# Performance work log

Hardware: AMD Instinct MI355X
Metric: run time of the kernel (lower is better)

The kernel has to match this reference:

```python
import jax, jax.numpy as jnp
import numpy as np

N = 64          # num_atoms
K = 2           # num_edge_types
VDIM = 32
EDIM = 32
HID = 64        # hard-coded n_hid in the module
B = 128         # num_sims
E = N * (N - 1)
_off = ~np.eye(N, dtype=bool)
SEND, RECV = [np.asarray(a) for a in np.where(_off)]  # edge e: node SEND[e] -> node RECV[e] (NRI: rel_send=rows, rel_rec=cols)
EPS = 1e-5  # torch BatchNorm1d default


def _mlp(x, W1, b1, W2, b2, gamma, beta):
    # NRI MLP: fc1 -> ELU -> fc2 -> ELU -> BatchNorm1d (training-mode batch stats over all but last dim)
    h = jax.nn.elu(x @ W1 + b1)
    o = jax.nn.elu(h @ W2 + b2)
    ax = tuple(range(o.ndim - 1))
    mu = o.mean(ax, keepdims=True)
    var = o.var(ax, keepdims=True)  # biased variance, as torch BN uses for normalization
    return gamma * (o - mu) * jax.lax.rsqrt(var + EPS) + beta


def setup_inputs():
    key = jax.random.key(0)
    ks = jax.random.split(key, 16)
    p = lambda k, shape: jax.random.normal(k, shape, jnp.float32) * 0.05
    return {
        "v0": jax.random.normal(ks[0], (B, N, VDIM), jnp.float32),
        "e0": jax.random.normal(ks[1], (B, N, N - 1, EDIM), jnp.float32),
        "edge_type": jax.random.uniform(ks[2], (B, E, K), dtype=jnp.float32),
        "mlpv_W1": p(ks[3], (EDIM, HID)), "mlpv_b1": p(ks[4], (HID,)),
        "mlpv_W2": p(ks[5], (HID, VDIM)), "mlpv_b2": p(ks[6], (VDIM,)),
        "mlpv_gamma": jnp.ones((VDIM,), jnp.float32), "mlpv_beta": jnp.zeros((VDIM,), jnp.float32),
        "mlpe_W1": p(ks[7], (K, 2 * VDIM, HID)), "mlpe_b1": p(ks[8], (K, HID)),
        "mlpe_W2": p(ks[9], (K, HID, EDIM)), "mlpe_b2": p(ks[10], (K, EDIM)),
        "mlpe_gamma": jnp.ones((K, EDIM), jnp.float32), "mlpe_beta": jnp.zeros((K, EDIM), jnp.float32),
    }


def reference(v0, e0, edge_type, mlpv_W1, mlpv_b1, mlpv_W2, mlpv_b2, mlpv_gamma, mlpv_beta,
              mlpe_W1, mlpe_b1, mlpe_W2, mlpe_b2, mlpe_gamma, mlpe_beta):
    e0f = e0.reshape(B, E, EDIM)
    # edge2node: rel_rec.T @ e0f is exactly a scatter-add of edge states onto receiver nodes, / num_atoms
    agg = jnp.zeros((B, N, EDIM), e0f.dtype).at[:, RECV].add(e0f) / N
    dv = _mlp(agg, mlpv_W1, mlpv_b1, mlpv_W2, mlpv_b2, mlpv_gamma, mlpv_beta)  # [B,N,VDIM]
    # node2edge: rel_rec@v0 / rel_send@v0 are gathers of node states per edge
    edges = jnp.concatenate([v0[:, RECV], v0[:, SEND]], axis=-1)  # [B,E,2V]
    # all K per-edge-type MLPs in one batched einsum (replaces the Python loop)
    h = jax.nn.elu(jnp.einsum('bef,kfh->bkeh', edges, mlpe_W1) + mlpe_b1[None, :, None, :])
    o = jax.nn.elu(jnp.einsum('bkeh,kho->bkeo', h, mlpe_W2) + mlpe_b2[None, :, None, :])
    mu = o.mean((0, 2), keepdims=True)   # BN stats per edge type, over (batch, edges)
    var = o.var((0, 2), keepdims=True)
    o = mlpe_gamma[None, :, None, :] * (o - mu) * jax.lax.rsqrt(var + EPS) + mlpe_beta[None, :, None, :]
    # mask each type's message by its edge_type weight, then sum over types
    de = (o * edge_type.transpose(0, 2, 1)[..., None]).sum(1)  # [B,E,EDIM]
    de = de.reshape(B, N, N - 1, EDIM)
    return (dv, de, edge_type * 0)
```

## Files before the change

kernel.cpp:

```cpp
#include <hip/hip_runtime.h>
#include <hip/hip_bf16.h>

#define NB 128
#define NA 64
#define NE 4032
#define KT 2
#define BE (NB * NE)
#define DV_SIZE 262144
#define DE_SIZE 16515072
#define ZERO_SIZE 1032192

#define PBLK_A 1008
#define TPW_A 8

#define EPI_EDGE_BLOCKS 8064
#define EPI_NODE_BLOCKS 1024

typedef __attribute__((ext_vector_type(8))) short short8;
typedef __attribute__((ext_vector_type(4))) float floatx4;

__device__ __forceinline__ float elu(float x) {
    return x > 0.0f ? x : __expf(x) - 1.0f;
}

__device__ __forceinline__ unsigned short f2bf(float x) {
    unsigned u = __float_as_uint(x);
    return (unsigned short)((u + 0x7FFFu + ((u >> 16) & 1u)) >> 16);
}

__device__ __forceinline__ unsigned pkbf(float a, float b) {
    __hip_bfloat162 h = __float22bfloat162_rn(make_float2(a, b));
    unsigned u;
    __builtin_memcpy(&u, &h, 4);
    return u;
}

__device__ __forceinline__ short8 pack8(float4 a, float4 b) {
    unsigned u[4] = {pkbf(a.x, a.y), pkbf(a.z, a.w), pkbf(b.x, b.y), pkbf(b.z, b.w)};
    short8 r;
    __builtin_memcpy(&r, u, 16);
    return r;
}

__global__ __launch_bounds__(256) void prep_kernel(const float* __restrict__ e0,
                                                   float* __restrict__ agg,
                                                   const float* __restrict__ v0,
                                                   unsigned short* __restrict__ v0bf) {
    if (blockIdx.x < 256) {
        const int f = blockIdx.x * 256 + threadIdx.x;
        const int c4 = f & 7;
        const int jn = (f >> 3) & 63;
        const int b = f >> 9;
        const float4* base = (const float4*)e0 + (size_t)b * 64 * 63 * 8;
        float x = 0.f, y = 0.f, z = 0.f, ww = 0.f;
#pragma unroll 8
        for (int i = 0; i < 64; i++) {
            int p = jn - (jn > i ? 1 : 0);
            p = p > 62 ? 62 : p;
            const float m = (i == jn) ? 0.0f : 1.0f;
            const float4 v = base[(i * 63 + p) * 8 + c4];
            x = fmaf(v.x, m, x);
            y = fmaf(v.y, m, y);
            z = fmaf(v.z, m, z);
            ww = fmaf(v.w, m, ww);
        }
        const float s = 1.0f / 64.0f;
        *(float4*)(agg + (size_t)f * 4) = make_float4(x * s, y * s, z * s, ww * s);
    } else {
        const int idx = (blockIdx.x - 256) * 256 + threadIdx.x;
        const float4 v = reinterpret_cast<const float4*>(v0)[idx];
        uint2 r;
        r.x = pkbf(v.x, v.y);
        r.y = pkbf(v.z, v.w);
        reinterpret_cast<uint2*>(v0bf)[idx] = r;
    }
}

struct SMW {
    short8 wA1[16][64];
    short8 wA2[8][64];
    float b1s[128];
    float b2s[64];
};
struct SME {
    SMW wk;
    unsigned hbuf[4][512];
};

__device__ __forceinline__ void stage_weights(SMW& sm, const float* __restrict__ W1,
                                              const float* __restrict__ b1,
                                              const float* __restrict__ W2,
                                              const float* __restrict__ b2) {
    const int tid = threadIdx.x;
#pragma unroll
    for (int s = 0; s < 4; s++) {
        const int slot = s * 256 + tid;
        const int f = slot >> 6, l = slot & 63;
        const int k = f >> 3, mt = (f >> 1) & 3, kf = f & 1;
        const int g = l >> 4, m15 = l & 15;
        short8 v;
#pragma unroll
        for (int j = 0; j < 8; j++) {
            const int kk = kf * 32 + g * 8 + j;
            v[j] = (short)f2bf(W1[(k * 64 + kk) * 64 + mt * 16 + m15]);
        }
        sm.wA1[f][l] = v;
    }
#pragma unroll
    for (int s = 0; s < 2; s++) {
        const int slot = s * 256 + tid;
        const int f = slot >> 6, l = slot & 63;
        const int k = f >> 2, mt2 = (f >> 1) & 1, kf = f & 1;
        const int g = l >> 4, m15 = l & 15;
        short8 v;
#pragma unroll
        for (int j = 0; j < 8; j++) {
            const int kk = kf * 32 + g * 8 + j;
            v[j] = (short)f2bf(W2[(k * 64 + kk) * 32 + mt2 * 16 + m15]);
        }
        sm.wA2[f][l] = v;
    }
    if (tid < 128) sm.b1s[tid] = b1[tid];
    if (tid < 64) sm.b2s[tid] = b2[tid];
}

__device__ __forceinline__ void load_xfrags(const unsigned short* __restrict__ v0bf,
                                            int row, int g, short8& bx0, short8& bx1) {
    const int b = row / NE;
    const int e = row - b * NE;
    const int i = e / 63;
    const int p = e - i * 63;
    const int j = p + (p >= i ? 1 : 0);
    bx0 = *(const short8*)(v0bf + ((b * 64 + j) * 32 + g * 8));
    bx1 = *(const short8*)(v0bf + ((b * 64 + i) * 32 + g * 8));
}

__global__ __launch_bounds__(256, 3) void edge_stats_mfma_kernel(
    const unsigned short* __restrict__ v0bf, const float* __restrict__ W1,
    const float* __restrict__ b1, const float* __restrict__ W2,
    const float* __restrict__ b2, float* __restrict__ buckets,
    unsigned short* __restrict__ o_e) {
    __shared__ SME sm;
    stage_weights(sm.wk, W1, b1, W2, b2);
    __syncthreads();

    const int lane = threadIdx.x & 63;
    const int w = threadIdx.x >> 6;
    const int g = lane >> 4, m15 = lane & 15;
    const int gw = blockIdx.x * 4 + w;
    unsigned* hw = &sm.hbuf[w][0];
    const int sw = m15 & 7;
    const int rbase = m15 * 32;

#pragma unroll 1
    for (int k = 0; k < 2; k++) {
        short8 a1r[4][2], a2r[2][2];
#pragma unroll
        for (int mt = 0; mt < 4; mt++)
#pragma unroll
            for (int kf = 0; kf < 2; kf++)
                a1r[mt][kf] = sm.wk.wA1[(k * 4 + mt) * 2 + kf][lane];
#pragma unroll
        for (int mt2 = 0; mt2 < 2; mt2++)
#pragma unroll
            for (int kf = 0; kf < 2; kf++)
                a2r[mt2][kf] = sm.wk.wA2[(k * 2 + mt2) * 2 + kf][lane];

        float st[2][4], sq[2][4];
#pragma unroll
        for (int m = 0; m < 2; m++)
#pragma unroll
            for (int r = 0; r < 4; r++) { st[m][r] = 0.f; sq[m][r] = 0.f; }

#pragma unroll 1
        for (int tt = 0; tt < TPW_A; tt++) {
            const int row = (gw * TPW_A + tt) * 16 + m15;
            short8 bx0, bx1;
            load_xfrags(v0bf, row, g, bx0, bx1);

#pragma unroll
            for (int mt = 0; mt < 4; mt++) {
                const float4 bb = *(const float4*)&sm.wk.b1s[k * 64 + mt * 16 + 4 * g];
                floatx4 acc = {bb.x, bb.y, bb.z, bb.w};
                acc = __builtin_amdgcn_mfma_f32_16x16x32_bf16(a1r[mt][0], bx0, acc, 0, 0, 0);
                acc = __builtin_amdgcn_mfma_f32_16x16x32_bf16(a1r[mt][1], bx1, acc, 0, 0, 0);
                uint2 hv;
                hv.x = pkbf(elu(acc[0]), elu(acc[1]));
                hv.y = pkbf(elu(acc[2]), elu(acc[3]));
                const int q = 2 * mt + (g >> 1);
                *(uint2*)&hw[rbase + ((q ^ sw) << 2) + 2 * (g & 1)] = hv;
            }
            const short8 bh0 = *(const short8*)&hw[rbase + (((g) ^ sw) << 2)];
            const short8 bh1 = *(const short8*)&hw[rbase + (((g + 4) ^ sw) << 2)];
#pragma unroll
            for (int mt2 = 0; mt2 < 2; mt2++) {
                const float4 bb = *(const float4*)&sm.wk.b2s[k * 32 + mt2 * 16 + 4 * g];
                floatx4 acc = {bb.x, bb.y, bb.z, bb.w};
                acc = __builtin_amdgcn_mfma_f32_16x16x32_bf16(a2r[mt2][0], bh0, acc, 0, 0, 0);
                acc = __builtin_amdgcn_mfma_f32_16x16x32_bf16(a2r[mt2][1], bh1, acc, 0, 0, 0);
                float v0v = elu(acc[0]), v1v = elu(acc[1]);
                float v2v = elu(acc[2]), v3v = elu(acc[3]);
                st[mt2][0] += v0v; sq[mt2][0] += v0v * v0v;
                st[mt2][1] += v1v; sq[mt2][1] += v1v * v1v;
                st[mt2][2] += v2v; sq[mt2][2] += v2v * v2v;
                st[mt2][3] += v3v; sq[mt2][3] += v3v * v3v;
                uint2 ov;
                ov.x = pkbf(v0v, v1v);
                ov.y = pkbf(v2v, v3v);
                *(uint2*)(o_e + ((size_t)k * BE + row) * 32 + mt2 * 16 + 4 * g) = ov;
            }
        }

        const int bk = gw & 31;
#pragma unroll
        for (int m = 0; m < 2; m++)
#pragma unroll
            for (int r = 0; r < 4; r++) {
                float s = st[m][r], ss = sq[m][r];
#pragma unroll
                for (int off = 1; off < 16; off <<= 1) {
                    s += __shfl_xor(s, off, 64);
                    ss += __shfl_xor(ss, off, 64);
                }
                if (m15 == 0) {
                    const int ch = m * 16 + 4 * g + r;
                    atomicAdd(&buckets[((bk * KT + k) * 32 + ch) * 2], s);
                    atomicAdd(&buckets[((bk * KT + k) * 32 + ch) * 2 + 1], ss);
                }
            }
    }
}

struct SMN {
    short8 wA1n[4][64];
    short8 wA2n[4][64];
    float b1s[64];
    float b2s[32];
    unsigned long long hbuf[4][16 * 20];
};

__global__ __launch_bounds__(256) void node_mlp_mfma_kernel(
    const float* __restrict__ agg, const float* __restrict__ W1,
    const float* __restrict__ b1, const float* __restrict__ W2,
    const float* __restrict__ b2, float* __restrict__ o_v,
    float* __restrict__ nbuckets) {
    __shared__ SMN sm;
    const int tid = threadIdx.x;
    {
        const int f = tid >> 6, l = tid & 63;
        const int g = l >> 4, m15 = l & 15;
        short8 v;
#pragma unroll
        for (int j = 0; j < 8; j++)
            v[j] = (short)f2bf(W1[(g * 8 + j) * 64 + f * 16 + m15]);
        sm.wA1n[f][l] = v;
        const int mt2 = f >> 1, kf = f & 1;
        short8 u;
#pragma unroll
        for (int j = 0; j < 8; j++)
            u[j] = (short)f2bf(W2[(kf * 32 + g * 8 + j) * 32 + mt2 * 16 + m15]);
        sm.wA2n[f][l] = u;
    }
    if (tid < 64) sm.b1s[tid] = b1[tid];
    else if (tid < 96) sm.b2s[tid - 64] = b2[tid - 64];
    __syncthreads();

    const int lane = tid & 63;
    const int w = tid >> 6;
    const int g = lane >> 4, m15 = lane & 15;
    const int tile = blockIdx.x * 4 + w;
    const int row = tile * 16 + m15;

    const float4* px = (const float4*)(agg + (size_t)row * 32 + g * 8);
    const short8 bx = pack8(px[0], px[1]);

    const char* hbase = (const char*)&sm.hbuf[w][0];
    unsigned long long* hw = &sm.hbuf[w][0];

#pragma unroll
    for (int mt = 0; mt < 4; mt++) {
        const float4 bb = *(const float4*)&sm.b1s[mt * 16 + 4 * g];
        floatx4 acc = {bb.x, bb.y, bb.z, bb.w};
        acc = __builtin_amdgcn_mfma_f32_16x16x32_bf16(sm.wA1n[mt][lane], bx, acc, 0, 0, 0);
        const unsigned lo = pkbf(elu(acc[0]), elu(acc[1]));
        const unsigned hi = pkbf(elu(acc[2]), elu(acc[3]));
        hw[m15 * 20 + mt * 4 + g] = ((unsigned long long)hi << 32) | lo;
    }
    const short8 bh0 = *(const short8*)(hbase + m15 * 160 + 0 + g * 16);
    const short8 bh1 = *(const short8*)(hbase + m15 * 160 + 64 + g * 16);

    const int bk = tile & 31;
#pragma unroll
    for (int mt2 = 0; mt2 < 2; mt2++) {
        const float4 bb = *(const float4*)&sm.b2s[mt2 * 16 + 4 * g];
        floatx4 acc = {bb.x, bb.y, bb.z, bb.w};
        acc = __builtin_amdgcn_mfma_f32_16x16x32_bf16(sm.wA2n[mt2 * 2 + 0][lane], bh0, acc, 0, 0, 0);
        acc = __builtin_amdgcn_mfma_f32_16x16x32_bf16(sm.wA2n[mt2 * 2 + 1][lane], bh1, acc, 0, 0, 0);
        float4 ov;
        ov.x = elu(acc[0]);
        ov.y = elu(acc[1]);
        ov.z = elu(acc[2]);
        ov.w = elu(acc[3]);
        *(float4*)(o_v + (size_t)row * 32 + mt2 * 16 + 4 * g) = ov;
        const float vv[4] = {ov.x, ov.y, ov.z, ov.w};
#pragma unroll
        for (int r = 0; r < 4; r++) {
            float s = vv[r], ss = vv[r] * vv[r];
#pragma unroll
            for (int off = 1; off < 16; off <<= 1) {
                s += __shfl_xor(s, off, 64);
                ss += __shfl_xor(ss, off, 64);
            }
            if (m15 == 0) {
                const int ch = mt2 * 16 + 4 * g + r;
                atomicAdd(&nbuckets[(bk * 32 + ch) * 2], s);
                atomicAdd(&nbuckets[(bk * 32 + ch) * 2 + 1], ss);
            }
        }
    }
}

__global__ __launch_bounds__(256) void epilogue_kernel(
    const unsigned short* __restrict__ o_e, const float* __restrict__ etype,
    const float* __restrict__ buckets, const float* __restrict__ ge,
    const float* __restrict__ bte, const float* __restrict__ o_v,
    const float* __restrict__ nbuckets, const float* __restrict__ gv,
    const float* __restrict__ btv, float* __restrict__ out) {
    __shared__ float afs[64], cfs[64];

    if (blockIdx.x < EPI_EDGE_BLOCKS) {
        if (threadIdx.x < 64) {
            const int k = threadIdx.x >> 5, c = threadIdx.x & 31;
            float s = 0.0f, ss = 0.0f;
#pragma unroll
            for (int bk = 0; bk < 32; bk++) {
                s += buckets[((bk * KT + k) * 32 + c) * 2];
                ss += buckets[((bk * KT + k) * 32 + c) * 2 + 1];
            }
            const float M = (float)BE;
            const float mu = s / M;
            const float var = ss / M - mu * mu;
            const float rs = rsqrtf(var + 1e-5f);
            const float af = ge[k * 32 + c] * rs;
            afs[threadIdx.x] = af;
            cfs[threadIdx.x] = bte[k * 32 + c] - mu * af;
        }
        __syncthreads();

        float* de = out + DV_SIZE;
        const int t = blockIdx.x * 256 + threadIdx.x;
        const int cg = t & 3;
        const int row = t >> 2;
        const uint4 p0 = *(const uint4*)(o_e + (size_t)row * 32 + cg * 8);
        const uint4 p1 = *(const uint4*)(o_e + ((size_t)BE + row) * 32 + cg * 8);
        const float2 wv = *(const float2*)(etype + (size_t)row * 2);
        const unsigned pu0[4] = {p0.x, p0.y, p0.z, p0.w};
        const unsigned pu1[4] = {p1.x, p1.y, p1.z, p1.w};

        float r[8];
#pragma unroll
        for (int u = 0; u < 8; u++) {
            const int ch = cg * 8 + u;
            const float o0 = __uint_as_float((u & 1) ? (pu0[u >> 1] & 0xFFFF0000u)
                                                     : (pu0[u >> 1] << 16));
            const float o1 = __uint_as_float((u & 1) ? (pu1[u >> 1] & 0xFFFF0000u)
                                                     : (pu1[u >> 1] << 16));
            r[u] = wv.x * fmaf(afs[ch], o0, cfs[ch]) +
                   wv.y * fmaf(afs[32 + ch], o1, cfs[32 + ch]);
        }
        float4* dst = (float4*)(de + (size_t)row * 32 + cg * 8);
        dst[0] = make_float4(r[0], r[1], r[2], r[3]);
        dst[1] = make_float4(r[4], r[5], r[6], r[7]);
    } else {
        if (threadIdx.x < 32) {
            const int c = threadIdx.x;
            float s = 0.0f, ss = 0.0f;
#pragma unroll
            for (int bk = 0; bk < 32; bk++) {
                s += nbuckets[(bk * 32 + c) * 2];
                ss += nbuckets[(bk * 32 + c) * 2 + 1];
            }
            const float M = 8192.0f;
            const float mu = s / M;
            const float var = ss / M - mu * mu;
            const float rs = rsqrtf(var + 1e-5f);
            const float af = gv[c] * rs;
            afs[c] = af;
            cfs[c] = btv[c] - mu * af;
        }
        __syncthreads();
        const int f = (blockIdx.x - EPI_EDGE_BLOCKS) * 256 + threadIdx.x;
        const int c = f & 31;
        out[f] = afs[c] * o_v[f] + cfs[c];
    }
}

extern "C" void kernel_launch(void* const* d_in, const int* in_sizes, int n_in,
                              void* d_out, int out_size, void* d_ws, size_t ws_size,
                              hipStream_t stream) {
    const float* v0 = (const float*)d_in[0];
    const float* e0 = (const float*)d_in[1];
    const float* etype = (const float*)d_in[2];
    const float* W1v = (const float*)d_in[3];
    const float* b1v = (const float*)d_in[4];
    const float* W2v = (const float*)d_in[5];
    const float* b2v = (const float*)d_in[6];
    const float* gv = (const float*)d_in[7];
    const float* btv = (const float*)d_in[8];
    const float* W1e = (const float*)d_in[9];
    const float* b1e = (const float*)d_in[10];
    const float* W2e = (const float*)d_in[11];
    const float* b2e = (const float*)d_in[12];
    const float* ge = (const float*)d_in[13];
    const float* bte = (const float*)d_in[14];
    float* out = (float*)d_out;

    float* ws = (float*)d_ws;
    float* buckets = ws;
    float* nbuckets = ws + 4096;
    float* agg = ws + 6144;
    float* o_v = ws + 268288;
    unsigned short* v0bf = (unsigned short*)(ws + 530432);
    unsigned short* o_e = (unsigned short*)(ws + 661504);

    hipMemsetAsync(buckets, 0, (4096 + 2048) * sizeof(float), stream);
    hipMemsetAsync(out + DV_SIZE + DE_SIZE, 0, ZERO_SIZE * sizeof(float), stream);

    prep_kernel<<<512, 256, 0, stream>>>(e0, agg, v0, v0bf);
    node_mlp_mfma_kernel<<<128, 256, 0, stream>>>(agg, W1v, b1v, W2v, b2v, o_v, nbuckets);
    edge_stats_mfma_kernel<<<PBLK_A, 256, 0, stream>>>(v0bf, W1e, b1e, W2e, b2e,
                                                       buckets, o_e);
    epilogue_kernel<<<EPI_EDGE_BLOCKS + EPI_NODE_BLOCKS, 256, 0, stream>>>(
        o_e, etype, buckets, ge, bte, o_v, nbuckets, gv, btv, out);
}
```

Measured before the change: 233.9 us.

## Fold memsets into kernels and parallelize edge-to-node aggregation across more blocks

```diff
diff --git a/kernel.cpp b/kernel.cpp
--- a/kernel.cpp
+++ b/kernel.cpp
@@ -15,6 +15,7 @@
 
 #define EPI_EDGE_BLOCKS 8064
 #define EPI_NODE_BLOCKS 1024
+#define EPI_ZERO_BLOCKS 1008
 
 typedef __attribute__((ext_vector_type(8))) short short8;
 typedef __attribute__((ext_vector_type(4))) float floatx4;
@@ -45,34 +46,45 @@
 __global__ __launch_bounds__(256) void prep_kernel(const float* __restrict__ e0,
                                                    float* __restrict__ agg,
                                                    const float* __restrict__ v0,
-                                                   unsigned short* __restrict__ v0bf) {
-    if (blockIdx.x < 256) {
-        const int f = blockIdx.x * 256 + threadIdx.x;
-        const int c4 = f & 7;
-        const int jn = (f >> 3) & 63;
-        const int b = f >> 9;
-        const float4* base = (const float4*)e0 + (size_t)b * 64 * 63 * 8;
-        float x = 0.f, y = 0.f, z = 0.f, ww = 0.f;
-#pragma unroll 8
-        for (int i = 0; i < 64; i++) {
-            int p = jn - (jn > i ? 1 : 0);
+                                                   unsigned short* __restrict__ v0bf,
+                                                   float* __restrict__ buckets) {
+    if (blockIdx.x < 8192) {
+        const int b = blockIdx.x >> 6, j = blockIdx.x & 63;
+        const int c = threadIdx.x & 31, ig = threadIdx.x >> 5;
+        const float* eb = e0 + (size_t)b * 64 * 63 * 32;
+        float s = 0.f;
+#pragma unroll
+        for (int t = 0; t < 8; t++) {
+            const int i = ig * 8 + t;
+            int p = j - (j > i ? 1 : 0);
             p = p > 62 ? 62 : p;
-            const float m = (i == jn) ? 0.0f : 1.0f;
-            const float4 v = base[(i * 63 + p) * 8 + c4];
-            x = fmaf(v.x, m, x);
-            y = fmaf(v.y, m, y);
-            z = fmaf(v.z, m, z);
-            ww = fmaf(v.w, m, ww);
-        }
-        const float s = 1.0f / 64.0f;
-        *(float4*)(agg + (size_t)f * 4) = make_float4(x * s, y * s, z * s, ww * s);
-    } else {
-        const int idx = (blockIdx.x - 256) * 256 + threadIdx.x;
+            const float m = (i == j) ? 0.0f : 1.0f;
+            s = fmaf(eb[(i * 63 + p) * 32 + c], m, s);
+        }
+        __shared__ float red[256];
+        red[threadIdx.x] = s;
+        __syncthreads();
+        if (threadIdx.x < 128) red[threadIdx.x] += red[threadIdx.x + 128];
+        __syncthreads();
+        if (threadIdx.x < 64) red[threadIdx.x] += red[threadIdx.x + 64];
+        __syncthreads();
+        if (threadIdx.x < 32) {
+            const float v = red[threadIdx.x] + red[threadIdx.x + 32];
+            agg[((size_t)b * 64 + j) * 32 + threadIdx.x] = v * (1.0f / 64.0f);
+        }
+    } else if (blockIdx.x < 8448) {
+        const int idx = (blockIdx.x - 8192) * 256 + threadIdx.x;
         const float4 v = reinterpret_cast<const float4*>(v0)[idx];
         uint2 r;
         r.x = pkbf(v.x, v.y);
         r.y = pkbf(v.z, v.w);
         reinterpret_cast<uint2*>(v0bf)[idx] = r;
+    } else {
+#pragma unroll
+        for (int it = 0; it < 6; it++) {
+            const int i4 = it * 256 + threadIdx.x;
+            *(float4*)(buckets + (size_t)i4 * 4) = make_float4(0.f, 0.f, 0.f, 0.f);
+        }
     }
 }
 
@@ -172,7 +184,7 @@
 #pragma unroll
             for (int r = 0; r < 4; r++) { st[m][r] = 0.f; sq[m][r] = 0.f; }
 
-#pragma unroll 1
+#pragma unroll 2
         for (int tt = 0; tt < TPW_A; tt++) {
             const int row = (gw * TPW_A + tt) * 16 + m15;
             short8 bx0, bx1;
@@ -371,7 +383,7 @@
         float4* dst = (float4*)(de + (size_t)row * 32 + cg * 8);
         dst[0] = make_float4(r[0], r[1], r[2], r[3]);
         dst[1] = make_float4(r[4], r[5], r[6], r[7]);
-    } else {
+    } else if (blockIdx.x < EPI_EDGE_BLOCKS + EPI_NODE_BLOCKS) {
         if (threadIdx.x < 32) {
             const int c = threadIdx.x;
             float s = 0.0f, ss = 0.0f;
@@ -392,6 +404,10 @@
         const int f = (blockIdx.x - EPI_EDGE_BLOCKS) * 256 + threadIdx.x;
         const int c = f & 31;
         out[f] = afs[c] * o_v[f] + cfs[c];
+    } else {
+        const int i4 = (blockIdx.x - EPI_EDGE_BLOCKS - EPI_NODE_BLOCKS) * 256 + threadIdx.x;
+        *(float4*)(out + DV_SIZE + DE_SIZE + (size_t)i4 * 4) =
+            make_float4(0.f, 0.f, 0.f, 0.f);
     }
 }
 
@@ -423,13 +439,10 @@
     unsigned short* v0bf = (unsigned short*)(ws + 530432);
     unsigned short* o_e = (unsigned short*)(ws + 661504);
 
-    hipMemsetAsync(buckets, 0, (4096 + 2048) * sizeof(float), stream);
-    hipMemsetAsync(out + DV_SIZE + DE_SIZE, 0, ZERO_SIZE * sizeof(float), stream);
-
-    prep_kernel<<<512, 256, 0, stream>>>(e0, agg, v0, v0bf);
+    prep_kernel<<<8449, 256, 0, stream>>>(e0, agg, v0, v0bf, buckets);
     node_mlp_mfma_kernel<<<128, 256, 0, stream>>>(agg, W1v, b1v, W2v, b2v, o_v, nbuckets);
     edge_stats_mfma_kernel<<<PBLK_A, 256, 0, stream>>>(v0bf, W1e, b1e, W2e, b2e,
                                                        buckets, o_e);
-    epilogue_kernel<<<EPI_EDGE_BLOCKS + EPI_NODE_BLOCKS, 256, 0, stream>>>(
+    epilogue_kernel<<<EPI_EDGE_BLOCKS + EPI_NODE_BLOCKS + EPI_ZERO_BLOCKS, 256, 0, stream>>>(
         o_e, etype, buckets, ge, bte, o_v, nbuckets, gv, btv, out);
 }
```

Result: no change. 229.9 us (-1.7%).

## Fold memsets and node MLP into existing kernels to cut launches

Applied to the files above, without the earlier changes.

```diff
diff --git a/kernel.cpp b/kernel.cpp
--- a/kernel.cpp
+++ b/kernel.cpp
@@ -12,9 +12,11 @@
 
 #define PBLK_A 1008
 #define TPW_A 8
+#define NODE_BLOCKS 128
 
 #define EPI_EDGE_BLOCKS 8064
 #define EPI_NODE_BLOCKS 1024
+#define EPI_ZERO_BLOCKS 1008
 
 typedef __attribute__((ext_vector_type(8))) short short8;
 typedef __attribute__((ext_vector_type(4))) float floatx4;
@@ -45,7 +47,8 @@
 __global__ __launch_bounds__(256) void prep_kernel(const float* __restrict__ e0,
                                                    float* __restrict__ agg,
                                                    const float* __restrict__ v0,
-                                                   unsigned short* __restrict__ v0bf) {
+                                                   unsigned short* __restrict__ v0bf,
+                                                   float* __restrict__ buckets) {
     if (blockIdx.x < 256) {
         const int f = blockIdx.x * 256 + threadIdx.x;
         const int c4 = f & 7;
@@ -66,13 +69,19 @@
         }
         const float s = 1.0f / 64.0f;
         *(float4*)(agg + (size_t)f * 4) = make_float4(x * s, y * s, z * s, ww * s);
-    } else {
+    } else if (blockIdx.x < 512) {
         const int idx = (blockIdx.x - 256) * 256 + threadIdx.x;
         const float4 v = reinterpret_cast<const float4*>(v0)[idx];
         uint2 r;
         r.x = pkbf(v.x, v.y);
         r.y = pkbf(v.z, v.w);
         reinterpret_cast<uint2*>(v0bf)[idx] = r;
+    } else {
+#pragma unroll
+        for (int it = 0; it < 6; it++) {
+            const int i4 = it * 256 + threadIdx.x;
+            *(float4*)(buckets + (size_t)i4 * 4) = make_float4(0.f, 0.f, 0.f, 0.f);
+        }
     }
 }
 
@@ -86,6 +95,17 @@
     SMW wk;
     unsigned hbuf[4][512];
 };
+struct SMN {
+    short8 wA1n[4][64];
+    short8 wA2n[4][64];
+    float b1s[64];
+    float b2s[32];
+    unsigned long long hbuf[4][16 * 20];
+};
+union SMU {
+    SME e;
+    SMN n;
+};
 
 __device__ __forceinline__ void stage_weights(SMW& sm, const float* __restrict__ W1,
                                               const float* __restrict__ b1,
@@ -139,182 +159,172 @@
     const unsigned short* __restrict__ v0bf, const float* __restrict__ W1,
     const float* __restrict__ b1, const float* __restrict__ W2,
     const float* __restrict__ b2, float* __restrict__ buckets,
-    unsigned short* __restrict__ o_e) {
-    __shared__ SME sm;
-    stage_weights(sm.wk, W1, b1, W2, b2);
-    __syncthreads();
-
+    unsigned short* __restrict__ o_e, const float* __restrict__ agg,
+    const float* __restrict__ W1v, const float* __restrict__ b1v,
+    const float* __restrict__ W2v, const float* __restrict__ b2v,
+    float* __restrict__ o_v, float* __restrict__ nbuckets) {
+    __shared__ SMU u;
     const int lane = threadIdx.x & 63;
     const int w = threadIdx.x >> 6;
     const int g = lane >> 4, m15 = lane & 15;
-    const int gw = blockIdx.x * 4 + w;
-    unsigned* hw = &sm.hbuf[w][0];
-    const int sw = m15 & 7;
-    const int rbase = m15 * 32;
+
+    if (blockIdx.x < PBLK_A) {
+        SME& sm = u.e;
+        stage_weights(sm.wk, W1, b1, W2, b2);
+        __syncthreads();
+
+        const int gw = blockIdx.x * 4 + w;
+        unsigned* hw = &sm.hbuf[w][0];
+        const int sw = m15 & 7;
+        const int rbase = m15 * 32;
 
 #pragma unroll 1
-    for (int k = 0; k < 2; k++) {
-        short8 a1r[4][2], a2r[2][2];
-#pragma unroll
-        for (int mt = 0; mt < 4; mt++)
-#pragma unroll
-            for (int kf = 0; kf < 2; kf++)
-                a1r[mt][kf] = sm.wk.wA1[(k * 4 + mt) * 2 + kf][lane];
-#pragma unroll
-        for (int mt2 = 0; mt2 < 2; mt2++)
-#pragma unroll
-            for (int kf = 0; kf < 2; kf++)
-                a2r[mt2][kf] = sm.wk.wA2[(k * 2 + mt2) * 2 + kf][lane];
-
-        float st[2][4], sq[2][4];
-#pragma unroll
-        for (int m = 0; m < 2; m++)
-#pragma unroll
-            for (int r = 0; r < 4; r++) { st[m][r] = 0.f; sq[m][r] = 0.f; }
-
-#pragma unroll 1
-        for (int tt = 0; tt < TPW_A; tt++) {
-            const int row = (gw * TPW_A + tt) * 16 + m15;
-            short8 bx0, bx1;
-            load_xfrags(v0bf, row, g, bx0, bx1);
-
-#pragma unroll
-            for (int mt = 0; mt < 4; mt++) {
-                const float4 bb = *(const float4*)&sm.wk.b1s[k * 64 + mt * 16 + 4 * g];
-                floatx4 acc = {bb.x, bb.y, bb.z, bb.w};
-                acc = __builtin_amdgcn_mfma_f32_16x16x32_bf16(a1r[mt][0], bx0, acc, 0, 0, 0);
-                acc = __builtin_amdgcn_mfma_f32_16x16x32_bf16(a1r[mt][1], bx1, acc, 0, 0, 0);
-                uint2 hv;
-                hv.x = pkbf(elu(acc[0]), elu(acc[1]));
-                hv.y = pkbf(elu(acc[2]), elu(acc[3]));
-                const int q = 2 * mt + (g >> 1);
-                *(uint2*)&hw[rbase + ((q ^ sw) << 2) + 2 * (g & 1)] = hv;
+        for (int k = 0; k < 2; k++) {
+            short8 a1r[4][2], a2r[2][2];
+#pragma unroll
+            for (int mt = 0; mt < 4; mt++)
+#pragma unroll
+                for (int kf = 0; kf < 2; kf++)
+                    a1r[mt][kf] = sm.wk.wA1[(k * 4 + mt) * 2 + kf][lane];
+#pragma unroll
+            for (int mt2 = 0; mt2 < 2; mt2++)
+#pragma unroll
+                for (int kf = 0; kf < 2; kf++)
+                    a2r[mt2][kf] = sm.wk.wA2[(k * 2 + mt2) * 2 + kf][lane];
+
+            float st[2][4], sq[2][4];
+#pragma unroll
+            for (int m = 0; m < 2; m++)
+#pragma unroll
+                for (int r = 0; r < 4; r++) { st[m][r] = 0.f; sq[m][r] = 0.f; }
+
+#pragma unroll 2
+            for (int tt = 0; tt < TPW_A; tt++) {
+                const int row = (gw * TPW_A + tt) * 16 + m15;
+                short8 bx0, bx1;
+                load_xfrags(v0bf, row, g, bx0, bx1);
+
+#pragma unroll
+                for (int mt = 0; mt < 4; mt++) {
+                    const float4 bb = *(const float4*)&sm.wk.b1s[k * 64 + mt * 16 + 4 * g];
+                    floatx4 acc = {bb.x, bb.y, bb.z, bb.w};
+                    acc = __builtin_amdgcn_mfma_f32_16x16x32_bf16(a1r[mt][0], bx0, acc, 0, 0, 0);
+                    acc = __builtin_amdgcn_mfma_f32_16x16x32_bf16(a1r[mt][1], bx1, acc, 0, 0, 0);
+                    uint2 hv;
+                    hv.x = pkbf(elu(acc[0]), elu(acc[1]));
+                    hv.y = pkbf(elu(acc[2]), elu(acc[3]));
+                    const int q = 2 * mt + (g >> 1);
+                    *(uint2*)&hw[rbase + ((q ^ sw) << 2) + 2 * (g & 1)] = hv;
+                }
+                const short8 bh0 = *(const short8*)&hw[rbase + (((g) ^ sw) << 2)];
+                const short8 bh1 = *(const short8*)&hw[rbase + (((g + 4) ^ sw) << 2)];
+#pragma unroll
+                for (int mt2 = 0; mt2 < 2; mt2++) {
+                    const float4 bb = *(const float4*)&sm.wk.b2s[k * 32 + mt2 * 16 + 4 * g];
+                    floatx4 acc = {bb.x, bb.y, bb.z, bb.w};
+                    acc = __builtin_amdgcn_mfma_f32_16x16x32_bf16(a2r[mt2][0], bh0, acc, 0, 0, 0);
+                    acc = __builtin_amdgcn_mfma_f32_16x16x32_bf16(a2r[mt2][1], bh1, acc, 0, 0, 0);
+                    float v0v = elu(acc[0]), v1v = elu(acc[1]);
+                    float v2v = elu(acc[2]), v3v = elu(acc[3]);
+                    st[mt2][0] += v0v; sq[mt2][0] += v0v * v0v;
+                    st[mt2][1] += v1v; sq[mt2][1] += v1v * v1v;
+                    st[mt2][2] += v2v; sq[mt2][2] += v2v * v2v;
+                    st[mt2][3] += v3v; sq[mt2][3] += v3v * v3v;
+                    uint2 ov;
+                    ov.x = pkbf(v0v, v1v);
+                    ov.y = pkbf(v2v, v3v);
+                    *(uint2*)(o_e + ((size_t)k * BE + row) * 32 + mt2 * 16 + 4 * g) = ov;
+                }
             }
-            const short8 bh0 = *(const short8*)&hw[rbase + (((g) ^ sw) << 2)];
-            const short8 bh1 = *(const short8*)&hw[rbase + (((g + 4) ^ sw) << 2)];
-#pragma unroll
-            for (int mt2 = 0; mt2 < 2; mt2++) {
-                const float4 bb = *(const float4*)&sm.wk.b2s[k * 32 + mt2 * 16 + 4 * g];
-                floatx4 acc = {bb.x, bb.y, bb.z, bb.w};
-                acc = __builtin_amdgcn_mfma_f32_16x16x32_bf16(a2r[mt2][0], bh0, acc, 0, 0, 0);
-                acc = __builtin_amdgcn_mfma_f32_16x16x32_bf16(a2r[mt2][1], bh1, acc, 0, 0, 0);
-                float v0v = elu(acc[0]), v1v = elu(acc[1]);
-                float v2v = elu(acc[2]), v3v = elu(acc[3]);
-                st[mt2][0] += v0v; sq[mt2][0] += v0v * v0v;
-                st[mt2][1] += v1v; sq[mt2][1] += v1v * v1v;
-                st[mt2][2] += v2v; sq[mt2][2] += v2v * v2v;
-                st[mt2][3] += v3v; sq[mt2][3] += v3v * v3v;
-                uint2 ov;
-                ov.x = pkbf(v0v, v1v);
-                ov.y = pkbf(v2v, v3v);
-                *(uint2*)(o_e + ((size_t)k * BE + row) * 32 + mt2 * 16 + 4 * g) = ov;
-            }
-        }
-
-        const int bk = gw & 31;
-#pragma unroll
-        for (int m = 0; m < 2; m++)
+
+            const int bk = gw & 31;
+#pragma unroll
+            for (int m = 0; m < 2; m++)
+#pragma unroll
+                for (int r = 0; r < 4; r++) {
+                    float s = st[m][r], ss = sq[m][r];
+#pragma unroll
+                    for (int off = 1; off < 16; off <<= 1) {
+                        s += __shfl_xor(s, off, 64);
+                        ss += __shfl_xor(ss, off, 64);
+                    }
+                    if (m15 == 0) {
+                        const int ch = m * 16 + 4 * g + r;
+                        atomicAdd(&buckets[((bk * KT + k) * 32 + ch) * 2], s);
+                        atomicAdd(&buckets[((bk * KT + k) * 32 + ch) * 2 + 1], ss);
+                    }
+                }
+        }
+    } else {
+        SMN& sm = u.n;
+        const int tid = threadIdx.x;
+        {
+            const int f = tid >> 6, l = tid & 63;
+            const int gg = l >> 4, mm = l & 15;
+            short8 v;
+#pragma unroll
+            for (int j = 0; j < 8; j++)
+                v[j] = (short)f2bf(W1v[(gg * 8 + j) * 64 + f * 16 + mm]);
+            sm.wA1n[f][l] = v;
+            const int mt2 = f >> 1, kf = f & 1;
+            short8 uu;
+#pragma unroll
+            for (int j = 0; j < 8; j++)
+                uu[j] = (short)f2bf(W2v[(kf * 32 + gg * 8 + j) * 32 + mt2 * 16 + mm]);
+            sm.wA2n[f][l] = uu;
+        }
+        if (tid < 64) sm.b1s[tid] = b1v[tid];
+        else if (tid < 96) sm.b2s[tid - 64] = b2v[tid - 64];
+        __syncthreads();
+
+        const int tile = (blockIdx.x - PBLK_A) * 4 + w;
+        const int row = tile * 16 + m15;
+
+        const float4* px = (const float4*)(agg + (size_t)row * 32 + g * 8);
+        const short8 bx = pack8(px[0], px[1]);
+
+        const char* hbase = (const char*)&sm.hbuf[w][0];
+        unsigned long long* hw = &sm.hbuf[w][0];
+
+#pragma unroll
+        for (int mt = 0; mt < 4; mt++) {
+            const float4 bb = *(const float4*)&sm.b1s[mt * 16 + 4 * g];
+            floatx4 acc = {bb.x, bb.y, bb.z, bb.w};
+            acc = __builtin_amdgcn_mfma_f32_16x16x32_bf16(sm.wA1n[mt][lane], bx, acc, 0, 0, 0);
+            const unsigned lo = pkbf(elu(acc[0]), elu(acc[1]));
+            const unsigned hi = pkbf(elu(acc[2]), elu(acc[3]));
+            hw[m15 * 20 + mt * 4 + g] = ((unsigned long long)hi << 32) | lo;
+        }
+        const short8 bh0 = *(const short8*)(hbase + m15 * 160 + 0 + g * 16);
+        const short8 bh1 = *(const short8*)(hbase + m15 * 160 + 64 + g * 16);
+
+        const int bk = tile & 31;
+#pragma unroll
+        for (int mt2 = 0; mt2 < 2; mt2++) {
+            const float4 bb = *(const float4*)&sm.b2s[mt2 * 16 + 4 * g];
+            floatx4 acc = {bb.x, bb.y, bb.z, bb.w};
+            acc = __builtin_amdgcn_mfma_f32_16x16x32_bf16(sm.wA2n[mt2 * 2 + 0][lane], bh0, acc, 0, 0, 0);
+            acc = __builtin_amdgcn_mfma_f32_16x16x32_bf16(sm.wA2n[mt2 * 2 + 1][lane], bh1, acc, 0, 0, 0);
+            float4 ov;
+            ov.x = elu(acc[0]);
+            ov.y = elu(acc[1]);
+            ov.z = elu(acc[2]);
+            ov.w = elu(acc[3]);
+            *(float4*)(o_v + (size_t)row * 32 + mt2 * 16 + 4 * g) = ov;
+            const float vv[4] = {ov.x, ov.y, ov.z, ov.w};
 #pragma unroll
             for (int r = 0; r < 4; r++) {
-                float s = st[m][r], ss = sq[m][r];
+                float s = vv[r], ss = vv[r] * vv[r];
 #pragma unroll
                 for (int off = 1; off < 16; off <<= 1) {
                     s += __shfl_xor(s, off, 64);
                     ss += __shfl_xor(ss, off, 64);
                 }
                 if (m15 == 0) {
-                    const int ch = m * 16 + 4 * g + r;
-                    atomicAdd(&buckets[((bk * KT + k) * 32 + ch) * 2], s);
-                    atomicAdd(&buckets[((bk * KT + k) * 32 + ch) * 2 + 1], ss);
+                    const int ch = mt2 * 16 + 4 * g + r;
+                    atomicAdd(&nbuckets[(bk * 32 + ch) * 2], s);
+                    atomicAdd(&nbuckets[(bk * 32 + ch) * 2 + 1], ss);
                 }
-            }
-    }
-}
-
-struct SMN {
-    short8 wA1n[4][64];
-    short8 wA2n[4][64];
-    float b1s[64];
-    float b2s[32];
-    unsigned long long hbuf[4][16 * 20];
-};
-
-__global__ __launch_bounds__(256) void node_mlp_mfma_kernel(
-    const float* __restrict__ agg, const float* __restrict__ W1,
-    const float* __restrict__ b1, const float* __restrict__ W2,
-    const float* __restrict__ b2, float* __restrict__ o_v,
-    float* __restrict__ nbuckets) {
-    __shared__ SMN sm;
-    const int tid = threadIdx.x;
-    {
-        const int f = tid >> 6, l = tid & 63;
-        const int g = l >> 4, m15 = l & 15;
-        short8 v;
-#pragma unroll
-        for (int j = 0; j < 8; j++)
-            v[j] = (short)f2bf(W1[(g * 8 + j) * 64 + f * 16 + m15]);
-        sm.wA1n[f][l] = v;
-        const int mt2 = f >> 1, kf = f & 1;
-        short8 u;
-#pragma unroll
-        for (int j = 0; j < 8; j++)
-            u[j] = (short)f2bf(W2[(kf * 32 + g * 8 + j) * 32 + mt2 * 16 + m15]);
-        sm.wA2n[f][l] = u;
-    }
-    if (tid < 64) sm.b1s[tid] = b1[tid];
-    else if (tid < 96) sm.b2s[tid - 64] = b2[tid - 64];
-    __syncthreads();
-
-    const int lane = tid & 63;
-    const int w = tid >> 6;
-    const int g = lane >> 4, m15 = lane & 15;
-    const int tile = blockIdx.x * 4 + w;
-    const int row = tile * 16 + m15;
-
-    const float4* px = (const float4*)(agg + (size_t)row * 32 + g * 8);
-    const short8 bx = pack8(px[0], px[1]);
-
-    const char* hbase = (const char*)&sm.hbuf[w][0];
-    unsigned long long* hw = &sm.hbuf[w][0];
-
-#pragma unroll
-    for (int mt = 0; mt < 4; mt++) {
-        const float4 bb = *(const float4*)&sm.b1s[mt * 16 + 4 * g];
-        floatx4 acc = {bb.x, bb.y, bb.z, bb.w};
-        acc = __builtin_amdgcn_mfma_f32_16x16x32_bf16(sm.wA1n[mt][lane], bx, acc, 0, 0, 0);
-        const unsigned lo = pkbf(elu(acc[0]), elu(acc[1]));
-        const unsigned hi = pkbf(elu(acc[2]), elu(acc[3]));
-        hw[m15 * 20 + mt * 4 + g] = ((unsigned long long)hi << 32) | lo;
-    }
-    const short8 bh0 = *(const short8*)(hbase + m15 * 160 + 0 + g * 16);
-    const short8 bh1 = *(const short8*)(hbase + m15 * 160 + 64 + g * 16);
-
-    const int bk = tile & 31;
-#pragma unroll
-    for (int mt2 = 0; mt2 < 2; mt2++) {
-        const float4 bb = *(const float4*)&sm.b2s[mt2 * 16 + 4 * g];
-        floatx4 acc = {bb.x, bb.y, bb.z, bb.w};
-        acc = __builtin_amdgcn_mfma_f32_16x16x32_bf16(sm.wA2n[mt2 * 2 + 0][lane], bh0, acc, 0, 0, 0);
-        acc = __builtin_amdgcn_mfma_f32_16x16x32_bf16(sm.wA2n[mt2 * 2 + 1][lane], bh1, acc, 0, 0, 0);
-        float4 ov;
-        ov.x = elu(acc[0]);
-        ov.y = elu(acc[1]);
-        ov.z = elu(acc[2]);
-        ov.w = elu(acc[3]);
-        *(float4*)(o_v + (size_t)row * 32 + mt2 * 16 + 4 * g) = ov;
-        const float vv[4] = {ov.x, ov.y, ov.z, ov.w};
-#pragma unroll
-        for (int r = 0; r < 4; r++) {
-            float s = vv[r], ss = vv[r] * vv[r];
-#pragma unroll
-            for (int off = 1; off < 16; off <<= 1) {
-                s += __shfl_xor(s, off, 64);
-                ss += __shfl_xor(ss, off, 64);
-            }
-            if (m15 == 0) {
-                const int ch = mt2 * 16 + 4 * g + r;
-                atomicAdd(&nbuckets[(bk * 32 + ch) * 2], s);
-                atomicAdd(&nbuckets[(bk * 32 + ch) * 2 + 1], ss);
             }
         }
     }
@@ -359,19 +369,19 @@
 
         float r[8];
 #pragma unroll
-        for (int u = 0; u < 8; u++) {
-            const int ch = cg * 8 + u;
-            const float o0 = __uint_as_float((u & 1) ? (pu0[u >> 1] & 0xFFFF0000u)
-                                                     : (pu0[u >> 1] << 16));
-            const float o1 = __uint_as_float((u & 1) ? (pu1[u >> 1] & 0xFFFF0000u)
-                                                     : (pu1[u >> 1] << 16));
-            r[u] = wv.x * fmaf(afs[ch], o0, cfs[ch]) +
-                   wv.y * fmaf(afs[32 + ch], o1, cfs[32 + ch]);
+        for (int uu = 0; uu < 8; uu++) {
+            const int ch = cg * 8 + uu;
+            const float o0 = __uint_as_float((uu & 1) ? (pu0[uu >> 1] & 0xFFFF0000u)
+                                                      : (pu0[uu >> 1] << 16));
+            const float o1 = __uint_as_float((uu & 1) ? (pu1[uu >> 1] & 0xFFFF0000u)
+                                                      : (pu1[uu >> 1] << 16));
+            r[uu] = wv.x * fmaf(afs[ch], o0, cfs[ch]) +
+                    wv.y * fmaf(afs[32 + ch], o1, cfs[32 + ch]);
         }
         float4* dst = (float4*)(de + (size_t)row * 32 + cg * 8);
         dst[0] = make_float4(r[0], r[1], r[2], r[3]);
         dst[1] = make_float4(r[4], r[5], r[6], r[7]);
-    } else {
+    } else if (blockIdx.x < EPI_EDGE_BLOCKS + EPI_NODE_BLOCKS) {
         if (threadIdx.x < 32) {
             const int c = threadIdx.x;
             float s = 0.0f, ss = 0.0f;
@@ -392,6 +402,10 @@
         const int f = (blockIdx.x - EPI_EDGE_BLOCKS) * 256 + threadIdx.x;
         const int c = f & 31;
         out[f] = afs[c] * o_v[f] + cfs[c];
+    } else {
+        const int i4 = (blockIdx.x - EPI_EDGE_BLOCKS - EPI_NODE_BLOCKS) * 256 + threadIdx.x;
+        *(float4*)(out + DV_SIZE + DE_SIZE + (size_t)i4 * 4) =
+            make_float4(0.f, 0.f, 0.f, 0.f);
     }
 }
 
@@ -423,13 +437,10 @@
     unsigned short* v0bf = (unsigned short*)(ws + 530432);
     unsigned short* o_e = (unsigned short*)(ws + 661504);
 
-    hipMemsetAsync(buckets, 0, (4096 + 2048) * sizeof(float), stream);
-    hipMemsetAsync(out + DV_SIZE + DE_SIZE, 0, ZERO_SIZE * sizeof(float), stream);
-
-    prep_kernel<<<512, 256, 0, stream>>>(e0, agg, v0, v0bf);
-    node_mlp_mfma_kernel<<<128, 256, 0, stream>>>(agg, W1v, b1v, W2v, b2v, o_v, nbuckets);
-    edge_stats_mfma_kernel<<<PBLK_A, 256, 0, stream>>>(v0bf, W1e, b1e, W2e, b2e,
-                                                       buckets, o_e);
-    epilogue_kernel<<<EPI_EDGE_BLOCKS + EPI_NODE_BLOCKS, 256, 0, stream>>>(
+    prep_kernel<<<513, 256, 0, stream>>>(e0, agg, v0, v0bf, buckets);
+    edge_stats_mfma_kernel<<<PBLK_A + NODE_BLOCKS, 256, 0, stream>>>(
+        v0bf, W1e, b1e, W2e, b2e, buckets, o_e,
+        agg, W1v, b1v, W2v, b2v, o_v, nbuckets);
+    epilogue_kernel<<<EPI_EDGE_BLOCKS + EPI_NODE_BLOCKS + EPI_ZERO_BLOCKS, 256, 0, stream>>>(
         o_e, etype, buckets, ge, bte, o_v, nbuckets, gv, btv, out);
 }
```

After: 226.6 us. 1.03x faster.
